# Performance work log

Measured on AMD Instinct MI355X. Metric: run time of the kernel, lower is better.

The kernel has to match this reference:

```python
import jax, jax.numpy as jnp
import numpy as np
from jax import lax

B, N, D, H = 8, 2048, 512, 1024


def setup_inputs() -> dict:
    key = jax.random.key(0)
    k0, k1, k2 = jax.random.split(key, 3)
    x = jax.random.normal(k0, (B, N, D), jnp.float32)
    conv_w = jax.random.normal(k1, (H, D, 3), jnp.float32) * (1.0 / np.sqrt(3 * D))
    conv_b = jnp.zeros((H,), jnp.float32)
    ln_g = jnp.ones((H,), jnp.float32)
    ln_b = jnp.zeros((H,), jnp.float32)
    proj_w = jax.random.normal(k2, (H, 2), jnp.float32) * (1.0 / np.sqrt(H))
    proj_b = jnp.zeros((2,), jnp.float32)
    return dict(x=x, conv_w=conv_w, conv_b=conv_b, ln_g=ln_g, ln_b=ln_b,
                proj_w=proj_w, proj_b=proj_b)


def reference(x, conv_w, conv_b, ln_g, ln_b, proj_w, proj_b):
    b, n, _ = x.shape
    # Conv1d(input_dim->hidden, k=3, pad=1) on [B, C, N]
    h = lax.conv_general_dilated(x.transpose(0, 2, 1), conv_w, (1,), [(1, 1)],
                                 dimension_numbers=('NCH', 'OIH', 'NCH'))
    h = h.transpose(0, 2, 1) + conv_b          # [B, N, H]
    h = jax.nn.relu(h)
    # LayerNorm over hidden dim (dropout is identity at inference)
    mu = jnp.mean(h, axis=-1, keepdims=True)
    var = jnp.mean((h - mu) ** 2, axis=-1, keepdims=True)
    h = (h - mu) * lax.rsqrt(var + 1e-5) * ln_g + ln_b
    groups_probs = h @ proj_w + proj_b          # [B, N, 2]

    g = jnp.argmax(groups_probs, axis=-1)       # [B, N] in {0,1}
    pos = jnp.arange(n)
    base = (pos + 1).astype(jnp.float32)        # 1..N
    # col 0 forced 0; start positions (g==1, pos>0) forced 0
    zero_mask = (pos[None, :] == 0) | ((g == 1) & (pos[None, :] > 0))
    vals = jnp.where(zero_mask, 0.0, jnp.broadcast_to(base[None, :], (b, n)))
    vals = vals.at[:, -1].set(float(n))         # last col = N (overrides zeroing)
    # stable descending sort by nonzero-ness == stable ascending sort by (val==0)
    order = jnp.argsort((vals == 0.0).astype(jnp.int32), axis=1)
    groups = jnp.take_along_axis(vals, order, axis=1)[:, :, None]  # [B, N, 1]

    t = base[None, None, :]                     # [1, 1, N], values 1..N
    # row 0: 1[t <= groups[:,0]]
    row0 = jnp.clip(groups[:, 0, :][:, None, :] - t + 1.0, 0.0, 1.0)      # [B, 1, N]
    # rows 1..: 1[groups[:,i-1] < t <= groups[:,i]]
    rest = (jnp.clip(groups[:, 1:, :] - t + 1.0, 0.0, 1.0)
            * jnp.clip(t - groups[:, :-1, :], 0.0, 1.0))                   # [B, N-1, N]
    grouping_matrix = jnp.concatenate([row0, rest], axis=1)                # [B, N, N]
    return (groups_probs, grouping_matrix)
```

## Files before the change

### kernel.cpp

```cpp
#include <hip/hip_runtime.h>

#define Bsz 8
#define Nsz 2048
#define Dsz 512
#define Hsz 1024
#define K3D 1536

typedef __attribute__((ext_vector_type(8))) short short8;
typedef __attribute__((ext_vector_type(4))) float f32x4;

static __device__ __forceinline__ unsigned short f2bf(float f) {
    unsigned u = __builtin_bit_cast(unsigned, f);
    unsigned r = (u + 0x7FFFu + ((u >> 16) & 1u)) >> 16;
    return (unsigned short)r;
}
static __device__ __forceinline__ float bf2f(unsigned short u) {
    return __builtin_bit_cast(float, (unsigned)u << 16);
}
static __device__ __forceinline__ void gld16(const void* g, void* l) {
    __builtin_amdgcn_global_load_lds(
        (const __attribute__((address_space(1))) void*)g,
        (__attribute__((address_space(3))) void*)l, 16, 0, 0);
}


__global__ __launch_bounds__(256) void prep_kernel(
    const float* __restrict__ cw, unsigned short* __restrict__ wsh,
    unsigned short* __restrict__ wsl,
    const float* __restrict__ lng, const float* __restrict__ lnb,
    const float* __restrict__ pw, float* __restrict__ CD,
    float* __restrict__ gq0, float* __restrict__ gq1)
{
    __shared__ float red[4][4];
    int blk = blockIdx.x, tid = threadIdx.x;
    if (blk < 192) {
        int gid = blk * 256 + tid;
        int s = gid >> 10, h = gid & 1023;
        int t = s >> 4, c = s & 15;
        const float* src = cw + (size_t)h * K3D + (size_t)c * 96 + t;
        short hv[32], lv[32];
        #pragma unroll
        for (int j = 0; j < 32; ++j) {
            float v = src[3 * j];
            unsigned short hi = f2bf(v);
            hv[j] = (short)hi;
            lv[j] = (short)f2bf(v - bf2f(hi));
        }
        #pragma unroll
        for (int m = 0; m < 4; ++m) {
            size_t dst = (((size_t)s * 4 + m) * 1024 + h) * 16;
            *(short8*)((char*)wsh + dst) = *(short8*)&hv[m * 8];
            *(short8*)((char*)wsl + dst) = *(short8*)&lv[m * 8];
        }
    } else if (blk == 192) {
        float c0 = 0.f, c1 = 0.f, d0 = 0.f, d1 = 0.f;
        for (int h = tid; h < Hsz; h += 256) {
            float g = lng[h], b = lnb[h];
            float w0 = pw[2 * h], w1 = pw[2 * h + 1];
            c0 = fmaf(g, w0, c0); c1 = fmaf(g, w1, c1);
            d0 = fmaf(b, w0, d0); d1 = fmaf(b, w1, d1);
        }
        #pragma unroll
        for (int m = 32; m >= 1; m >>= 1) {
            c0 += __shfl_xor(c0, m, 64); c1 += __shfl_xor(c1, m, 64);
            d0 += __shfl_xor(d0, m, 64); d1 += __shfl_xor(d1, m, 64);
        }
        int w = tid >> 6;
        if ((tid & 63) == 0) { red[w][0] = c0; red[w][1] = c1; red[w][2] = d0; red[w][3] = d1; }
        __syncthreads();
        if (tid == 0) {
            CD[0] = red[0][0] + red[1][0] + red[2][0] + red[3][0];
            CD[1] = red[0][1] + red[1][1] + red[2][1] + red[3][1];
            CD[2] = red[0][2] + red[1][2] + red[2][2] + red[3][2];
            CD[3] = red[0][3] + red[1][3] + red[2][3] + red[3][3];
        }
    } else {
        int h = (blk - 193) * 256 + tid;
        float g = lng[h];
        gq0[h] = g * pw[2 * h];
        gq1[h] = g * pw[2 * h + 1];
    }
}

__global__ __launch_bounds__(256) void convert_x_kernel(
    const float* __restrict__ x, unsigned short* __restrict__ xsh,
    unsigned short* __restrict__ xsl)
{
    int tid = threadIdx.x;
    int r = blockIdx.x * 4 + (tid >> 6);
    int e = tid & 63;
    int b  = r / 2050;
    int rp = r - b * 2050;
    int c  = e >> 2;
    int qq = e & 3;
    size_t dst = ((((size_t)b * 16 + c) * 4 + qq) * 2050 + rp) * 16;
    short8 hv, lv;
    if (rp == 0 || rp == 2049) {
        #pragma unroll
        for (int u = 0; u < 8; ++u) { hv[u] = 0; lv[u] = 0; }
    } else {
        const float* p = x + ((size_t)b * Nsz + (rp - 1)) * Dsz + e * 8;
        float4 v0 = *(const float4*)p;
        float4 v1 = *(const float4*)(p + 4);
        float vv[8] = { v0.x, v0.y, v0.z, v0.w, v1.x, v1.y, v1.z, v1.w };
        #pragma unroll
        for (int u = 0; u < 8; ++u) {
            unsigned short h = f2bf(vv[u]);
            hv[u] = (short)h;
            lv[u] = (short)f2bf(vv[u] - bf2f(h));
        }
    }
    *(short8*)((char*)xsh + dst) = hv;
    *(short8*)((char*)xsl + dst) = lv;
}

__global__ __launch_bounds__(512, 2) void gemm9_kernel(
    const unsigned short* __restrict__ xsh, const unsigned short* __restrict__ xsl,
    const unsigned short* __restrict__ wsh, const unsigned short* __restrict__ wsl,
    const float* __restrict__ cb, const float* __restrict__ gq0,
    const float* __restrict__ gq1, float* __restrict__ part)
{
    __shared__ __align__(16) char lds[65536];

    int tid = threadIdx.x;
    int bid = blockIdx.x;
    int xcd = bid & 7, idx = bid >> 3;
    int mt  = (xcd >> 1) * 16 + (idx >> 1);
    int ntb = (xcd & 1) * 2 + (idx & 1);
    int bb  = mt >> 3;
    int n0  = (mt & 7) * 256;
    int n0c = ntb * 256;
    int n0g = bb * Nsz + (mt & 7) * 256;

    int l = tid & 63, w = tid >> 6;
    int wr = w >> 2, wc = w & 3;
    int r = l & 15, qq = l >> 4;
    int aoff_r = qq * 4096 + (wr * 128 + r) * 16;

    const char* pA = (const char*)(w < 4 ? xsh : xsl)
                   + (size_t)bb * 2099200 + (w & 3) * 32800 + (size_t)(n0 + l) * 16;
    int ldsAw = ((w & 4) ? 16384 : 0) + (w & 3) * 4096;

    const char* pBh = (const char*)wsh + qq * 16384 + (size_t)(n0c + wc * 64 + r) * 16;
    const char* pBl = (const char*)wsl + qq * 16384 + (size_t)(n0c + wc * 64 + r) * 16;

    f32x4 acc[8][4];
    #pragma unroll
    for (int i = 0; i < 8; ++i)
        #pragma unroll
        for (int j = 0; j < 4; ++j) acc[i][j] = (f32x4){0.f, 0.f, 0.f, 0.f};

    short8 bh0[4], bl0[4], bh1[4], bl1[4];

#define LOADB(BH, BL, sn) do { size_t o = (size_t)(sn) * 65536;                \
    _Pragma("unroll") for (int j = 0; j < 4; ++j) {                            \
        BH[j] = *(const short8*)(pBh + o + j * 256);                           \
        BL[j] = *(const short8*)(pBl + o + j * 256); } } while (0)

#define STAGEA(lb, sn) do {                                                    \
    size_t ao = (size_t)(((sn) & 15) * 131200 + ((sn) >> 4) * 16);             \
    _Pragma("unroll") for (int g = 0; g < 4; ++g)                              \
        gld16(pA + ao + g * 1024, (lb) + ldsAw + g * 1024); } while (0)

#define COMPUTE(buf, BH, BL) do {                                              \
    _Pragma("unroll") for (int mh = 0; mh < 2; ++mh) {                         \
        short8 ah[4], al[4];                                                   \
        _Pragma("unroll") for (int i = 0; i < 4; ++i) {                        \
            ah[i] = *(const short8*)((buf) + aoff_r + (mh * 4 + i) * 256);     \
            al[i] = *(const short8*)((buf) + 16384 + aoff_r + (mh * 4 + i) * 256); } \
        __builtin_amdgcn_s_setprio(1);                                         \
        _Pragma("unroll") for (int i = 0; i < 4; ++i)                          \
            _Pragma("unroll") for (int j = 0; j < 4; ++j) {                    \
                acc[mh*4+i][j] = __builtin_amdgcn_mfma_f32_16x16x32_bf16(ah[i], BH[j], acc[mh*4+i][j], 0, 0, 0); \
                acc[mh*4+i][j] = __builtin_amdgcn_mfma_f32_16x16x32_bf16(ah[i], BL[j], acc[mh*4+i][j], 0, 0, 0); \
                acc[mh*4+i][j] = __builtin_amdgcn_mfma_f32_16x16x32_bf16(al[i], BH[j], acc[mh*4+i][j], 0, 0, 0); } \
        __builtin_amdgcn_s_setprio(0);                                         \
    } } while (0)

    LOADB(bh0, bl0, 0);
    STAGEA(lds, 0);

    for (int sp = 0; sp < 24; ++sp) {
        int s0 = sp * 2, s1 = s0 + 1;
        LOADB(bh1, bl1, s1);
        STAGEA(lds + 32768, s1);
        asm volatile("s_waitcnt vmcnt(12)" ::: "memory");
        __builtin_amdgcn_s_barrier();
        COMPUTE(lds, bh0, bl0);
        __builtin_amdgcn_s_barrier();
        if (s1 < 47) {
            LOADB(bh0, bl0, s1 + 1);
            STAGEA(lds, s1 + 1);
            asm volatile("s_waitcnt vmcnt(12)" ::: "memory");
        } else {
            asm volatile("s_waitcnt vmcnt(0)" ::: "memory");
        }
        __builtin_amdgcn_s_barrier();
        COMPUTE(lds + 32768, bh1, bl1);
        __builtin_amdgcn_s_barrier();
    }
#undef LOADB
#undef STAGEA
#undef COMPUTE

    float cbv[4], g0v[4], g1v[4];
    #pragma unroll
    for (int j = 0; j < 4; ++j) {
        int col = n0c + wc * 64 + j * 16 + r;
        cbv[j] = cb[col]; g0v[j] = gq0[col]; g1v[j] = gq1[col];
    }
    int slot = ntb * 16 + wc * 4;
    #pragma unroll
    for (int m = 0; m < 8; ++m) {
        #pragma unroll
        for (int reg = 0; reg < 4; ++reg) {
            float v0 = 0.f, v2 = 0.f, va = 0.f, vb = 0.f;
            #pragma unroll
            for (int j = 0; j < 4; ++j) {
                float v = acc[m][j][reg] + cbv[j];
                v = fmaxf(v, 0.f);
                v0 += v;
                v2 = fmaf(v, v, v2);
                va = fmaf(v, g0v[j], va);
                vb = fmaf(v, g1v[j], vb);
            }
            #pragma unroll
            for (int msk = 1; msk < 16; msk <<= 1) {
                v0 += __shfl_xor(v0, msk, 64); v2 += __shfl_xor(v2, msk, 64);
                va += __shfl_xor(va, msk, 64); vb += __shfl_xor(vb, msk, 64);
            }
            if (r == 0) {
                int rowg = n0g + wr * 128 + m * 16 + qq * 4 + reg;
                *(f32x4*)(part + (size_t)rowg * 64 + slot) = (f32x4){v0, v2, va, vb};
            }
        }
    }
}

__global__ __launch_bounds__(256) void probs_kernel(
    const float* __restrict__ part, const float* __restrict__ CD,
    const float* __restrict__ pb, float* __restrict__ probs,
    int* __restrict__ gout)
{
    int row = blockIdx.x * 256 + threadIdx.x;
    float S0 = 0.f, S2 = 0.f, Sa = 0.f, Sb = 0.f;
    const float4* p = (const float4*)(part + (size_t)row * 64);
    #pragma unroll
    for (int c = 0; c < 16; ++c) {
        float4 v = p[c];
        S0 += v.x; S2 += v.y; Sa += v.z; Sb += v.w;
    }
    float mu  = S0 * (1.0f / Hsz);
    float var = S2 * (1.0f / Hsz) - mu * mu;
    float rsq = 1.0f / sqrtf(var + 1e-5f);
    float p0 = fmaf(rsq, Sa - mu * CD[0], CD[2] + pb[0]);
    float p1 = fmaf(rsq, Sb - mu * CD[1], CD[3] + pb[1]);
    probs[(size_t)row * 2]     = p0;
    probs[(size_t)row * 2 + 1] = p1;
    gout[row] = (p1 > p0) ? 1 : 0;
}

#define ROWS 64
#define CCH 128
#define NCC (Hsz / CCH)
#define DSTEP 32

__global__ __launch_bounds__(256) void consts_kernel(
    const float* __restrict__ lng, const float* __restrict__ lnb,
    const float* __restrict__ pw, float* __restrict__ CD)
{
    int tid = threadIdx.x;
    float c0 = 0.f, c1 = 0.f, d0 = 0.f, d1 = 0.f;
    for (int h = tid; h < Hsz; h += 256) {
        float g = lng[h], b = lnb[h];
        float w0 = pw[2 * h], w1 = pw[2 * h + 1];
        c0 = fmaf(g, w0, c0); c1 = fmaf(g, w1, c1);
        d0 = fmaf(b, w0, d0); d1 = fmaf(b, w1, d1);
    }
    #pragma unroll
    for (int m = 32; m >= 1; m >>= 1) {
        c0 += __shfl_xor(c0, m, 64); c1 += __shfl_xor(c1, m, 64);
        d0 += __shfl_xor(d0, m, 64); d1 += __shfl_xor(d1, m, 64);
    }
    __shared__ float red[4][4];
    int w = tid >> 6;
    if ((tid & 63) == 0) { red[w][0] = c0; red[w][1] = c1; red[w][2] = d0; red[w][3] = d1; }
    __syncthreads();
    if (tid == 0) {
        CD[0] = red[0][0] + red[1][0] + red[2][0] + red[3][0];
        CD[1] = red[0][1] + red[1][1] + red[2][1] + red[3][1];
        CD[2] = red[0][2] + red[1][2] + red[2][2] + red[3][2];
        CD[3] = red[0][3] + red[1][3] + red[2][3] + red[3][3];
    }
}

__global__ __launch_bounds__(256) void conv_ln_proj_kernel(
    const float* __restrict__ x, const float* __restrict__ cw,
    const float* __restrict__ cb, const float* __restrict__ lng,
    const float* __restrict__ pw, const float* __restrict__ pb,
    const float* __restrict__ CD, float* __restrict__ probs,
    int* __restrict__ gout)
{
    __shared__ float Xl[DSTEP][66];
    __shared__ float Bl[3][DSTEP][CCH];
    __shared__ float Sl[ROWS][4];

    int tid = threadIdx.x;
    int blk = blockIdx.x;
    int b  = blk >> 5;
    int n0 = (blk & 31) * ROWS;
    int rg = tid >> 5;
    int cg = tid & 31;
    int sr = tid >> 2;
    int sq = tid & 3;
    const float* xb = x + (size_t)b * Nsz * Dsz;

    float s0[8], s2[8], sa[8], sb[8];
    #pragma unroll
    for (int i = 0; i < 8; ++i) { s0[i] = 0.f; s2[i] = 0.f; sa[i] = 0.f; sb[i] = 0.f; }

    for (int cc = 0; cc < NCC; ++cc) {
        float cbv[4], gq0[4], gq1[4];
        {
            int hb = cc * CCH + cg * 4;
            #pragma unroll
            for (int j = 0; j < 4; ++j) {
                int h = hb + j;
                cbv[j] = cb[h];
                float gg = lng[h];
                gq0[j] = gg * pw[2 * h];
                gq1[j] = gg * pw[2 * h + 1];
            }
        }
        float acc[8][4];
        #pragma unroll
        for (int i = 0; i < 8; ++i)
            #pragma unroll
            for (int j = 0; j < 4; ++j) acc[i][j] = 0.f;

        for (int ds = 0; ds < Dsz / DSTEP; ++ds) {
            int d0 = ds * DSTEP;
            __syncthreads();
            {
                int n = n0 - 1 + sr;
                float4 v0 = make_float4(0.f, 0.f, 0.f, 0.f), v1 = v0;
                if ((unsigned)n < (unsigned)Nsz) {
                    const float* p = xb + (size_t)n * Dsz + d0 + sq * 8;
                    v0 = *(const float4*)p;
                    v1 = *(const float4*)(p + 4);
                }
                int dd = sq * 8;
                Xl[dd + 0][sr] = v0.x; Xl[dd + 1][sr] = v0.y;
                Xl[dd + 2][sr] = v0.z; Xl[dd + 3][sr] = v0.w;
                Xl[dd + 4][sr] = v1.x; Xl[dd + 5][sr] = v1.y;
                Xl[dd + 6][sr] = v1.z; Xl[dd + 7][sr] = v1.w;
                if (tid < 8) {
                    int r2 = 64 + (tid >> 2);
                    int q2 = tid & 3;
                    int n2 = n0 - 1 + r2;
                    float4 u0 = make_float4(0.f, 0.f, 0.f, 0.f), u1 = u0;
                    if ((unsigned)n2 < (unsigned)Nsz) {
                        const float* p2 = xb + (size_t)n2 * Dsz + d0 + q2 * 8;
                        u0 = *(const float4*)p2;
                        u1 = *(const float4*)(p2 + 4);
                    }
                    int dd2 = q2 * 8;
                    Xl[dd2 + 0][r2] = u0.x; Xl[dd2 + 1][r2] = u0.y;
                    Xl[dd2 + 2][r2] = u0.z; Xl[dd2 + 3][r2] = u0.w;
                    Xl[dd2 + 4][r2] = u1.x; Xl[dd2 + 5][r2] = u1.y;
                    Xl[dd2 + 6][r2] = u1.z; Xl[dd2 + 7][r2] = u1.w;
                }
            }
            {
                int hl = tid >> 1;
                int half = tid & 1;
                const float* p = cw + (size_t)(cc * CCH + hl) * K3D + (size_t)d0 * 3 + half * 48;
                #pragma unroll
                for (int mq = 0; mq < 12; ++mq) {
                    float4 v = *(const float4*)(p + mq * 4);
                    float vv[4] = { v.x, v.y, v.z, v.w };
                    #pragma unroll
                    for (int e = 0; e < 4; ++e) {
                        int c  = mq * 4 + e;
                        int dl = half * 16 + c / 3;
                        int kk = c % 3;
                        Bl[kk][dl][hl] = vv[e];
                    }
                }
            }
            __syncthreads();
            #pragma unroll 4
            for (int dd = 0; dd < DSTEP; ++dd) {
                float a[10];
                #pragma unroll
                for (int j = 0; j < 10; ++j) a[j] = Xl[dd][rg * 8 + j];
                #pragma unroll
                for (int kk = 0; kk < 3; ++kk) {
                    float4 bv = *(const float4*)&Bl[kk][dd][cg * 4];
                    #pragma unroll
                    for (int i = 0; i < 8; ++i) {
                        float av = a[i + kk];
                        acc[i][0] = fmaf(av, bv.x, acc[i][0]);
                        acc[i][1] = fmaf(av, bv.y, acc[i][1]);
                        acc[i][2] = fmaf(av, bv.z, acc[i][2]);
                        acc[i][3] = fmaf(av, bv.w, acc[i][3]);
                    }
                }
            }
        }
        #pragma unroll
        for (int i = 0; i < 8; ++i) {
            #pragma unroll
            for (int j = 0; j < 4; ++j) {
                float v = acc[i][j] + cbv[j];
                v = fmaxf(v, 0.f);
                s0[i] += v;
                s2[i] = fmaf(v, v, s2[i]);
                sa[i] = fmaf(v, gq0[j], sa[i]);
                sb[i] = fmaf(v, gq1[j], sb[i]);
            }
        }
    }
    #pragma unroll
    for (int i = 0; i < 8; ++i) {
        float v0 = s0[i], v2 = s2[i], va = sa[i], vb = sb[i];
        #pragma unroll
        for (int mm = 16; mm >= 1; mm >>= 1) {
            v0 += __shfl_xor(v0, mm, 64); v2 += __shfl_xor(v2, mm, 64);
            va += __shfl_xor(va, mm, 64); vb += __shfl_xor(vb, mm, 64);
        }
        if (cg == 0) {
            int rr = rg * 8 + i;
            Sl[rr][0] = v0; Sl[rr][1] = v2; Sl[rr][2] = va; Sl[rr][3] = vb;
        }
    }
    __syncthreads();
    if (tid < ROWS) {
        int rr = tid, n = n0 + rr;
        float S0 = Sl[rr][0], S2 = Sl[rr][1], Sa = Sl[rr][2], Sb = Sl[rr][3];
        float mu  = S0 * (1.0f / Hsz);
        float var = S2 * (1.0f / Hsz) - mu * mu;
        float rsq = 1.0f / sqrtf(var + 1e-5f);
        float p0 = fmaf(rsq, Sa - mu * CD[0], CD[2] + pb[0]);
        float p1 = fmaf(rsq, Sb - mu * CD[1], CD[3] + pb[1]);
        size_t ro = (size_t)(b * Nsz + n);
        probs[ro * 2]     = p0;
        probs[ro * 2 + 1] = p1;
        gout[ro] = (p1 > p0) ? 1 : 0;
    }
}

__global__ __launch_bounds__(256) void bounds_kernel(
    const int* __restrict__ g, float* __restrict__ vlist, int* __restrict__ Kb)
{
    int b = blockIdx.x, tid = threadIdx.x;
    int base = tid * 8;
    int f[8]; float val[8]; int lsum = 0;
    #pragma unroll
    for (int u = 0; u < 8; ++u) {
        int i = base + u;
        int nz;
        if (i == Nsz - 1) nz = 1;
        else if (i == 0)  nz = 0;
        else              nz = (g[b * Nsz + i] == 0) ? 1 : 0;
        f[u] = nz;
        val[u] = (i == Nsz - 1) ? (float)Nsz : (float)(i + 1);
        lsum += nz;
    }
    int lane = tid & 63, w = tid >> 6;
    int sc = lsum;
    #pragma unroll
    for (int off = 1; off < 64; off <<= 1) {
        int t = __shfl_up(sc, off, 64);
        if (lane >= off) sc += t;
    }
    __shared__ int wsum[4];
    if (lane == 63) wsum[w] = sc;
    __syncthreads();
    int woff = 0;
    #pragma unroll
    for (int k = 0; k < 4; ++k) if (k < w) woff += wsum[k];
    int pos = woff + (sc - lsum);
    #pragma unroll
    for (int u = 0; u < 8; ++u) {
        if (f[u]) { vlist[b * Nsz + pos] = val[u]; pos++; }
    }
    if (tid == 255) Kb[b] = woff + sc;
}

__global__ __launch_bounds__(256) void fill_kernel(
    const float* __restrict__ vlist, const int* __restrict__ Kb,
    float* __restrict__ mat)
{
    int blk = blockIdx.x;
    int b = blk >> 11, j = blk & 2047;
    int K = Kb[b];
    float c = (j < K) ? vlist[b * Nsz + j] : 0.0f;
    float a = (j == 0) ? 0.0f : vlist[b * Nsz + j - 1];
    int tc = threadIdx.x * 8;
    float o[8];
    #pragma unroll
    for (int e = 0; e < 8; ++e) {
        float t = (float)(tc + e + 1);
        o[e] = (t > a && t <= c) ? 1.0f : 0.0f;
    }
    float4* p = (float4*)(mat + (size_t)blk * Nsz + tc);
    p[0] = make_float4(o[0], o[1], o[2], o[3]);
    p[1] = make_float4(o[4], o[5], o[6], o[7]);
}

extern "C" void kernel_launch(void* const* d_in, const int* in_sizes, int n_in,
                              void* d_out, int out_size, void* d_ws, size_t ws_size,
                              hipStream_t stream)
{
    const float* x      = (const float*)d_in[0];
    const float* conv_w = (const float*)d_in[1];
    const float* conv_b = (const float*)d_in[2];
    const float* ln_g   = (const float*)d_in[3];
    const float* ln_b   = (const float*)d_in[4];
    const float* proj_w = (const float*)d_in[5];
    const float* proj_b = (const float*)d_in[6];

    float* out = (float*)d_out;
    char*  wsb = (char*)d_ws;

    size_t cur = 0;
    auto take = [&](size_t b) { size_t r = cur; cur = (cur + b + 255) & ~(size_t)255; return r; };
    size_t oCD  = take(16);
    size_t oGQ0 = take(Hsz * 4);
    size_t oGQ1 = take(Hsz * 4);
    size_t oKb  = take(32);
    size_t oG   = take((size_t)Bsz * Nsz * 4);
    size_t oV   = take((size_t)Bsz * Nsz * 4);
    size_t oPart= take((size_t)Bsz * Nsz * 64 * 4);
    size_t oXh  = take((size_t)Bsz * 16 * 4 * 2050 * 16);
    size_t oXl  = take((size_t)Bsz * 16 * 4 * 2050 * 16);
    size_t oWh  = take((size_t)48 * 4 * 1024 * 16);
    size_t oWl  = take((size_t)48 * 4 * 1024 * 16);
    bool fast = ws_size >= cur;

    if (fast) {
        float* CD    = (float*)(wsb + oCD);
        float* gq0   = (float*)(wsb + oGQ0);
        float* gq1   = (float*)(wsb + oGQ1);
        int*   Kb    = (int*)  (wsb + oKb);
        int*   g     = (int*)  (wsb + oG);
        float* vlist = (float*)(wsb + oV);
        float* part  = (float*)(wsb + oPart);
        unsigned short* xsh = (unsigned short*)(wsb + oXh);
        unsigned short* xsl = (unsigned short*)(wsb + oXl);
        unsigned short* wsh = (unsigned short*)(wsb + oWh);
        unsigned short* wsl = (unsigned short*)(wsb + oWl);

        prep_kernel<<<197, 256, 0, stream>>>(conv_w, wsh, wsl, ln_g, ln_b, proj_w, CD, gq0, gq1);
        convert_x_kernel<<<Bsz * 2050 / 4, 256, 0, stream>>>(x, xsh, xsl);
        gemm9_kernel<<<256, 512, 0, stream>>>(
            xsh, xsl, wsh, wsl, conv_b, gq0, gq1, part);
        probs_kernel<<<Bsz * Nsz / 256, 256, 0, stream>>>(part, CD, proj_b, out, g);
        bounds_kernel<<<Bsz, 256, 0, stream>>>(g, vlist, Kb);
        fill_kernel<<<Bsz * Nsz, 256, 0, stream>>>(vlist, Kb, out + (size_t)Bsz * Nsz * 2);
    } else {
        float* wf  = (float*)d_ws;
        int*   wi  = (int*)d_ws;
        float* CD    = wf;
        int*   Kb    = wi + 4;
        int*   g     = wi + 16;
        float* vlist = wf + 16 + Bsz * Nsz;

        consts_kernel<<<1, 256, 0, stream>>>(ln_g, ln_b, proj_w, CD);
        conv_ln_proj_kernel<<<Bsz * Nsz / ROWS, 256, 0, stream>>>(
            x, conv_w, conv_b, ln_g, proj_w, proj_b, CD, out, g);
        bounds_kernel<<<Bsz, 256, 0, stream>>>(g, vlist, Kb);
        fill_kernel<<<Bsz * Nsz, 256, 0, stream>>>(vlist, Kb, out + (size_t)Bsz * Nsz * 2);
    }
}
```

Measured before the change: 187.8 us.

## Retile conv GEMM to 128x128 blocks with A in registers, B staged in LDS

Replaces the 256x256-tile, 512-thread GEMM with a 128x128-tile, 256-thread kernel on a 1024-block grid. The roles swap: activations (A) now stream straight into registers and the weight tile (B) is staged through LDS. The block swizzle is changed to match, and the epilogue writes 8 partial slots per row instead of 16. This aims for more blocks per CU and a smaller LDS footprint, at the cost of more global reloads of A and W across the smaller tiles. The part buffer still has 64 floats per row, with slots now ntb*8+wc*4.

```diff
diff --git a/kernel.cpp b/kernel.cpp
--- a/kernel.cpp
+++ b/kernel.cpp
@@ -114,93 +114,99 @@
     *(short8*)((char*)xsl + dst) = lv;
 }
 
-__global__ __launch_bounds__(512, 2) void gemm9_kernel(
+__global__ __launch_bounds__(256, 2) void gemm10_kernel(
     const unsigned short* __restrict__ xsh, const unsigned short* __restrict__ xsl,
     const unsigned short* __restrict__ wsh, const unsigned short* __restrict__ wsl,
     const float* __restrict__ cb, const float* __restrict__ gq0,
     const float* __restrict__ gq1, float* __restrict__ part)
 {
-    __shared__ __align__(16) char lds[65536];
+    __shared__ __align__(16) char lds[32768];
 
     int tid = threadIdx.x;
-    int bid = blockIdx.x;
-    int xcd = bid & 7, idx = bid >> 3;
-    int mt  = (xcd >> 1) * 16 + (idx >> 1);
-    int ntb = (xcd & 1) * 2 + (idx & 1);
-    int bb  = mt >> 3;
-    int n0  = (mt & 7) * 256;
-    int n0c = ntb * 256;
-    int n0g = bb * Nsz + (mt & 7) * 256;
+    int swz = (blockIdx.x & 7) * 128 + (blockIdx.x >> 3);
+    int mt  = swz >> 3;
+    int ntb = swz & 7;
+    int bb  = mt >> 4;
+    int n0  = (mt & 15) * 128;
+    int n0c = ntb * 128;
+    int n0g = bb * Nsz + n0;
 
     int l = tid & 63, w = tid >> 6;
-    int wr = w >> 2, wc = w & 3;
+    int wr = w >> 1, wc = w & 1;
     int r = l & 15, qq = l >> 4;
-    int aoff_r = qq * 4096 + (wr * 128 + r) * 16;
-
-    const char* pA = (const char*)(w < 4 ? xsh : xsl)
-                   + (size_t)bb * 2099200 + (w & 3) * 32800 + (size_t)(n0 + l) * 16;
-    int ldsAw = ((w & 4) ? 16384 : 0) + (w & 3) * 4096;
-
-    const char* pBh = (const char*)wsh + qq * 16384 + (size_t)(n0c + wc * 64 + r) * 16;
-    const char* pBl = (const char*)wsl + qq * 16384 + (size_t)(n0c + wc * 64 + r) * 16;
-
-    f32x4 acc[8][4];
-    #pragma unroll
-    for (int i = 0; i < 8; ++i)
+
+    int boff_r = qq * 2048 + (wc * 64 + r) * 16;
+    int ldsBw  = w * 2048;
+
+    const char* pBh = (const char*)wsh + w * 16384 + (size_t)(n0c + l) * 16;
+    const char* pBl = (const char*)wsl + w * 16384 + (size_t)(n0c + l) * 16;
+
+    const char* pAh = (const char*)xsh + (size_t)bb * 2099200 + qq * 32800
+                    + (size_t)(n0 + wr * 64 + r) * 16;
+    const char* pAl = (const char*)xsl + (size_t)bb * 2099200 + qq * 32800
+                    + (size_t)(n0 + wr * 64 + r) * 16;
+
+    f32x4 acc[4][4];
+    #pragma unroll
+    for (int i = 0; i < 4; ++i)
         #pragma unroll
         for (int j = 0; j < 4; ++j) acc[i][j] = (f32x4){0.f, 0.f, 0.f, 0.f};
 
-    short8 bh0[4], bl0[4], bh1[4], bl1[4];
-
-#define LOADB(BH, BL, sn) do { size_t o = (size_t)(sn) * 65536;                \
+    short8 a0h[4], a0l[4], a1h[4], a1l[4];
+
+#define AOFF(sn) ((size_t)(((sn) & 15) * 131200 + ((sn) >> 4) * 16))
+#define LOADA(AH, AL, sn) do { size_t ao = AOFF(sn);                           \
+    _Pragma("unroll") for (int f = 0; f < 4; ++f) {                            \
+        AH[f] = *(const short8*)(pAh + ao + f * 256);                          \
+        AL[f] = *(const short8*)(pAl + ao + f * 256); } } while (0)
+
+#define STAGEB(lb, sn) do { size_t bo = (size_t)(sn) * 65536;                  \
+    gld16(pBh + bo,        (lb) + ldsBw);                                      \
+    gld16(pBh + bo + 1024, (lb) + ldsBw + 1024);                               \
+    gld16(pBl + bo,        (lb) + 8192 + ldsBw);                               \
+    gld16(pBl + bo + 1024, (lb) + 8192 + ldsBw + 1024); } while (0)
+
+#define COMPUTE(buf, AH, AL) do {                                              \
+    short8 bh[4], bl[4];                                                       \
     _Pragma("unroll") for (int j = 0; j < 4; ++j) {                            \
-        BH[j] = *(const short8*)(pBh + o + j * 256);                           \
-        BL[j] = *(const short8*)(pBl + o + j * 256); } } while (0)
-
-#define STAGEA(lb, sn) do {                                                    \
-    size_t ao = (size_t)(((sn) & 15) * 131200 + ((sn) >> 4) * 16);             \
-    _Pragma("unroll") for (int g = 0; g < 4; ++g)                              \
-        gld16(pA + ao + g * 1024, (lb) + ldsAw + g * 1024); } while (0)
-
-#define COMPUTE(buf, BH, BL) do {                                              \
-    _Pragma("unroll") for (int mh = 0; mh < 2; ++mh) {                         \
-        short8 ah[4], al[4];                                                   \
-        _Pragma("unroll") for (int i = 0; i < 4; ++i) {                        \
-            ah[i] = *(const short8*)((buf) + aoff_r + (mh * 4 + i) * 256);     \
-            al[i] = *(const short8*)((buf) + 16384 + aoff_r + (mh * 4 + i) * 256); } \
-        __builtin_amdgcn_s_setprio(1);                                         \
-        _Pragma("unroll") for (int i = 0; i < 4; ++i)                          \
-            _Pragma("unroll") for (int j = 0; j < 4; ++j) {                    \
-                acc[mh*4+i][j] = __builtin_amdgcn_mfma_f32_16x16x32_bf16(ah[i], BH[j], acc[mh*4+i][j], 0, 0, 0); \
-                acc[mh*4+i][j] = __builtin_amdgcn_mfma_f32_16x16x32_bf16(ah[i], BL[j], acc[mh*4+i][j], 0, 0, 0); \
-                acc[mh*4+i][j] = __builtin_amdgcn_mfma_f32_16x16x32_bf16(al[i], BH[j], acc[mh*4+i][j], 0, 0, 0); } \
-        __builtin_amdgcn_s_setprio(0);                                         \
-    } } while (0)
-
-    LOADB(bh0, bl0, 0);
-    STAGEA(lds, 0);
+        bh[j] = *(const short8*)((buf) + boff_r + j * 256);                    \
+        bl[j] = *(const short8*)((buf) + 8192 + boff_r + j * 256); }           \
+    __builtin_amdgcn_s_setprio(1);                                             \
+    _Pragma("unroll") for (int i = 0; i < 4; ++i)                              \
+        _Pragma("unroll") for (int j = 0; j < 4; ++j) {                        \
+            acc[i][j] = __builtin_amdgcn_mfma_f32_16x16x32_bf16(AH[i], bh[j], acc[i][j], 0, 0, 0); \
+            acc[i][j] = __builtin_amdgcn_mfma_f32_16x16x32_bf16(AH[i], bl[j], acc[i][j], 0, 0, 0); \
+            acc[i][j] = __builtin_amdgcn_mfma_f32_16x16x32_bf16(AL[i], bh[j], acc[i][j], 0, 0, 0); } \
+    __builtin_amdgcn_s_setprio(0);                                             \
+} while (0)
+
+    LOADA(a0h, a0l, 0);
+    STAGEB(lds, 0);
 
     for (int sp = 0; sp < 24; ++sp) {
-        int s0 = sp * 2, s1 = s0 + 1;
-        LOADB(bh1, bl1, s1);
-        STAGEA(lds + 32768, s1);
+        int s1 = sp * 2 + 1;
+        LOADA(a1h, a1l, s1);
+        STAGEB(lds + 16384, s1);
         asm volatile("s_waitcnt vmcnt(12)" ::: "memory");
         __builtin_amdgcn_s_barrier();
-        COMPUTE(lds, bh0, bl0);
+        asm volatile("" ::: "memory");
+        COMPUTE(lds, a0h, a0l);
         __builtin_amdgcn_s_barrier();
         if (s1 < 47) {
-            LOADB(bh0, bl0, s1 + 1);
-            STAGEA(lds, s1 + 1);
+            LOADA(a0h, a0l, s1 + 1);
+            STAGEB(lds, s1 + 1);
             asm volatile("s_waitcnt vmcnt(12)" ::: "memory");
         } else {
             asm volatile("s_waitcnt vmcnt(0)" ::: "memory");
         }
         __builtin_amdgcn_s_barrier();
-        COMPUTE(lds + 32768, bh1, bl1);
+        asm volatile("" ::: "memory");
+        COMPUTE(lds + 16384, a1h, a1l);
         __builtin_amdgcn_s_barrier();
     }
-#undef LOADB
-#undef STAGEA
+#undef AOFF
+#undef LOADA
+#undef STAGEB
 #undef COMPUTE
 
     float cbv[4], g0v[4], g1v[4];
@@ -209,15 +215,15 @@
         int col = n0c + wc * 64 + j * 16 + r;
         cbv[j] = cb[col]; g0v[j] = gq0[col]; g1v[j] = gq1[col];
     }
-    int slot = ntb * 16 + wc * 4;
-    #pragma unroll
-    for (int m = 0; m < 8; ++m) {
+    int slot = ntb * 8 + wc * 4;
+    #pragma unroll
+    for (int i = 0; i < 4; ++i) {
         #pragma unroll
         for (int reg = 0; reg < 4; ++reg) {
             float v0 = 0.f, v2 = 0.f, va = 0.f, vb = 0.f;
             #pragma unroll
             for (int j = 0; j < 4; ++j) {
-                float v = acc[m][j][reg] + cbv[j];
+                float v = acc[i][j][reg] + cbv[j];
                 v = fmaxf(v, 0.f);
                 v0 += v;
                 v2 = fmaf(v, v, v2);
@@ -230,7 +236,7 @@
                 va += __shfl_xor(va, msk, 64); vb += __shfl_xor(vb, msk, 64);
             }
             if (r == 0) {
-                int rowg = n0g + wr * 128 + m * 16 + qq * 4 + reg;
+                int rowg = n0g + wr * 64 + i * 16 + qq * 4 + reg;
                 *(f32x4*)(part + (size_t)rowg * 64 + slot) = (f32x4){v0, v2, va, vb};
             }
         }
@@ -554,7 +560,7 @@
 
         prep_kernel<<<197, 256, 0, stream>>>(conv_w, wsh, wsl, ln_g, ln_b, proj_w, CD, gq0, gq1);
         convert_x_kernel<<<Bsz * 2050 / 4, 256, 0, stream>>>(x, xsh, xsl);
-        gemm9_kernel<<<256, 512, 0, stream>>>(
+        gemm10_kernel<<<1024, 256, 0, stream>>>(
             xsh, xsl, wsh, wsl, conv_b, gq0, gq1, part);
         probs_kernel<<<Bsz * Nsz / 256, 256, 0, stream>>>(part, CD, proj_b, out, g);
         bounds_kernel<<<Bsz, 256, 0, stream>>>(g, vlist, Kb);
```

After: 187.1 us (median of 2 runs). Within noise of the previous version (-0.4%).
